# Kernel tuning notes

Hardware: AMD Instinct MI355X
Metric: run time of the kernel (lower is better)

Reference implementation:

```python
import jax, jax.numpy as jnp
import numpy as np

N, E = 50000, 800000
IN, HID, OUT = 128, 256, 128
BN_EPS = 1e-5


def setup_inputs() -> dict:
    key = jax.random.key(0)
    ks = jax.random.split(key, 12)
    x = jax.random.normal(ks[0], (N, IN), dtype=jnp.float32)
    edge_index = jax.random.randint(ks[1], (2, E), 0, N, dtype=jnp.int64)
    edge_weight = jax.random.uniform(ks[2], (E,), dtype=jnp.float32)
    # GCNConv weights (glorot-ish scale) and biases
    W0 = jax.random.normal(ks[3], (IN, HID), dtype=jnp.float32) * (1.0 / np.sqrt(IN))
    b0 = jnp.zeros((HID,), jnp.float32)
    W1 = jax.random.normal(ks[4], (HID, HID), dtype=jnp.float32) * (1.0 / np.sqrt(HID))
    b1 = jnp.zeros((HID,), jnp.float32)
    Wl = jax.random.normal(ks[5], (HID, OUT), dtype=jnp.float32) * (1.0 / np.sqrt(HID))
    bl = jnp.zeros((OUT,), jnp.float32)
    # BatchNorm affine params (eval mode: running_mean=0, running_var=1)
    g0 = 1.0 + 0.1 * jax.random.normal(ks[6], (HID,), dtype=jnp.float32)
    be0 = 0.1 * jax.random.normal(ks[7], (HID,), dtype=jnp.float32)
    g1 = 1.0 + 0.1 * jax.random.normal(ks[8], (HID,), dtype=jnp.float32)
    be1 = 0.1 * jax.random.normal(ks[9], (HID,), dtype=jnp.float32)
    return {"x": x, "edge_index": edge_index, "edge_weight": edge_weight,
            "W0": W0, "b0": b0, "W1": W1, "b1": b1, "Wl": Wl, "bl": bl,
            "g0": g0, "be0": be0, "g1": g1, "be1": be1}


def reference(x, edge_index, edge_weight, W0, b0, W1, b1, Wl, bl, g0, be0, g1, be1):
    n = x.shape[0]
    row, col = edge_index[0], edge_index[1]
    # add self-loops with weight 1 (GCNConv default)
    ar = jnp.arange(n)
    rowf = jnp.concatenate([row, ar])
    colf = jnp.concatenate([col, ar])
    wf = jnp.concatenate([edge_weight, jnp.ones((n,), x.dtype)])
    # symmetric normalization: D^{-1/2} A D^{-1/2}
    deg = jax.ops.segment_sum(wf, colf, num_segments=n)
    dinv = jnp.where(deg > 0, jax.lax.rsqrt(deg), 0.0)
    norm = dinv[rowf] * wf * dinv[colf]  # [E+N]

    def conv(h, W, b):
        h = h @ W                       # [n, d_out]
        msg = h[rowf] * norm[:, None]   # gather + scale per edge
        return jax.ops.segment_sum(msg, colf, num_segments=n) + b

    def bn_eval(h, g, b):
        # eval-mode BN with running_mean=0, running_var=1
        return h * (g / jnp.sqrt(1.0 + BN_EPS)) + b

    h = jax.nn.relu(bn_eval(conv(x, W0, b0), g0, be0))
    h = jax.nn.relu(bn_eval(conv(h, W1, b1), g1, be1))
    h = conv(h, Wl, bl)
    return jax.nn.log_softmax(h, axis=1)
```

## Files before the change

kernel.cpp:

```cpp
#include <hip/hip_runtime.h>
#include <cstddef>
#include <cstdint>


#define GCN_BN_EPS 1e-5f
#define NB_CHUNK 64
#define NPART 4

typedef short v8bf __attribute__((ext_vector_type(8)));
typedef float v4f __attribute__((ext_vector_type(4)));


__device__ __forceinline__ float4 unpack_bf4(uint2 u) {
  float4 r;
  r.x = __uint_as_float(u.x << 16);
  r.y = __uint_as_float(u.x & 0xffff0000u);
  r.z = __uint_as_float(u.y << 16);
  r.w = __uint_as_float(u.y & 0xffff0000u);
  return r;
}
__device__ __forceinline__ uint16_t f2bf(float f) {
  uint32_t u = __float_as_uint(f);
  return (uint16_t)((u + 0x7fffu + ((u >> 16) & 1u)) >> 16);
}
__device__ __forceinline__ uint2 pack_bf4(float4 v) {
  uint2 r;
  r.x = (uint32_t)f2bf(v.x) | ((uint32_t)f2bf(v.y) << 16);
  r.y = (uint32_t)f2bf(v.z) | ((uint32_t)f2bf(v.w) << 16);
  return r;
}


__global__ void detect_kernel(const int* __restrict__ ei, int* __restrict__ flag) {
  if (threadIdx.x == 0) {
    int nz = 0;
    for (int k = 1; k < 64; k += 2) nz |= ei[k];
    *flag = (nz == 0) ? 1 : 0;
  }
}

__global__ void decode_kernel(const int* __restrict__ ei, const float* __restrict__ ew,
                              const int* __restrict__ flag,
                              int* __restrict__ col_, uint2* __restrict__ pk, int E) {
  int e = blockIdx.x * blockDim.x + threadIdx.x;
  if (e >= E) return;
  int r, c;
  if (*flag) { r = ei[2 * e]; c = ei[2 * (E + e)]; }
  else       { r = ei[e];     c = ei[E + e]; }
  col_[e] = c;
  pk[e] = make_uint2((unsigned)r, __float_as_uint(ew[e]));
}

__global__ __launch_bounds__(256) void hist_kernel(const int* __restrict__ col_,
                                                   int* __restrict__ hist,
                                                   int E, int n) {
  extern __shared__ unsigned int hsh[];
  const int chunk = blockIdx.x, part = blockIdx.y;
  const int npl = (n + NPART - 1) / NPART;
  const int lo = part * npl, hi = min(lo + npl, n);
  const int nw = (npl + 1) >> 1;
  for (int i = threadIdx.x; i < nw; i += 256) hsh[i] = 0u;
  __syncthreads();
  const int per = (E + NB_CHUNK - 1) / NB_CHUNK;
  const int e0 = chunk * per, e1 = min(e0 + per, E);
  for (int e = e0 + threadIdx.x; e < e1; e += 256) {
    int c = col_[e];
    if (c >= lo && c < hi) {
      int cl = c - lo;
      atomicAdd(&hsh[cl >> 1], 1u << ((cl & 1) * 16));
    }
  }
  __syncthreads();
  for (int i = threadIdx.x; i < hi - lo; i += 256)
    hist[(size_t)chunk * n + lo + i] = (int)((hsh[i >> 1] >> ((i & 1) * 16)) & 0xffffu);
}

__global__ __launch_bounds__(256) void scan1_kernel(const int* __restrict__ hist,
                                                    int* __restrict__ cnt,
                                                    int* __restrict__ bsum, int n) {
  __shared__ int ws[4];
  int i = blockIdx.x * 256 + threadIdx.x;
  int v = 0;
  if (i < n) {
    for (int b = 0; b < NB_CHUNK; ++b) v += hist[(size_t)b * n + i];
    cnt[i] = v;
  }
  int x = v;
#pragma unroll
  for (int s = 1; s < 64; s <<= 1) x += __shfl_xor(x, s, 64);
  if ((threadIdx.x & 63) == 0) ws[threadIdx.x >> 6] = x;
  __syncthreads();
  if (threadIdx.x == 0) bsum[blockIdx.x] = ws[0] + ws[1] + ws[2] + ws[3];
}

__global__ __launch_bounds__(1024) void scan2_kernel(int* __restrict__ bsum, int G,
                                                     int* __restrict__ off, int n, int E) {
  __shared__ int wsum[16], woff[16];
  int tid = threadIdx.x, lane = tid & 63, wv = tid >> 6;
  int v = (tid < G) ? bsum[tid] : 0;
  int x = v;
#pragma unroll
  for (int s = 1; s < 64; s <<= 1) { int t = __shfl_up(x, s, 64); if (lane >= s) x += t; }
  if (lane == 63) wsum[wv] = x;
  __syncthreads();
  if (wv == 0) {
    int wsv = (lane < 16) ? wsum[lane] : 0;
    int y = wsv;
#pragma unroll
    for (int s = 1; s < 16; s <<= 1) { int t = __shfl_up(y, s, 64); if (lane >= s) y += t; }
    if (lane < 16) woff[lane] = y - wsv;
  }
  __syncthreads();
  if (tid < G) bsum[tid] = x - v + woff[wv];
  if (tid == 0) off[n] = E;
}

__global__ __launch_bounds__(256) void scan3_kernel(const int* __restrict__ cnt,
                                                    const int* __restrict__ bsum,
                                                    int* __restrict__ off, int n) {
  __shared__ int wsum[4], woff[4];
  int tid = threadIdx.x, lane = tid & 63, wv = tid >> 6;
  int i = blockIdx.x * 256 + tid;
  int v = (i < n) ? cnt[i] : 0;
  int x = v;
#pragma unroll
  for (int s = 1; s < 64; s <<= 1) { int t = __shfl_up(x, s, 64); if (lane >= s) x += t; }
  if (lane == 63) wsum[wv] = x;
  __syncthreads();
  if (tid == 0) { int r = 0; for (int k = 0; k < 4; ++k) { woff[k] = r; r += wsum[k]; } }
  __syncthreads();
  if (i < n) off[i] = x - v + woff[wv] + bsum[blockIdx.x];
}

__global__ void base_kernel(const int* __restrict__ off, int* __restrict__ hist, int n) {
  int i = blockIdx.x * blockDim.x + threadIdx.x;
  if (i >= n) return;
  int run = off[i];
  for (int b = 0; b < NB_CHUNK; ++b) {
    size_t idx = (size_t)b * n + i;
    int h = hist[idx];
    hist[idx] = run;
    run += h;
  }
}

__global__ __launch_bounds__(256) void fill_kernel(
    const int* __restrict__ col_, const uint2* __restrict__ pk,
    const int* __restrict__ base, uint2* __restrict__ csr, int E, int n) {
  extern __shared__ int cur[];
  const int chunk = blockIdx.x, part = blockIdx.y;
  const int npl = (n + NPART - 1) / NPART;
  const int lo = part * npl, hi = min(lo + npl, n);
  for (int i = threadIdx.x; i < hi - lo; i += 256)
    cur[i] = base[(size_t)chunk * n + lo + i];
  __syncthreads();
  const int per = (E + NB_CHUNK - 1) / NB_CHUNK;
  const int e0 = chunk * per, e1 = min(e0 + per, E);
  for (int e = e0 + threadIdx.x; e < e1; e += 256) {
    int c = col_[e];
    if (c >= lo && c < hi) {
      int p = atomicAdd(&cur[c - lo], 1);
      csr[p] = pk[e];
    }
  }
}

__global__ void degdinv_kernel(const int* __restrict__ off, const uint2* __restrict__ csr,
                               float* __restrict__ dinv, int n) {
  int i = blockIdx.x * blockDim.x + threadIdx.x;
  if (i >= n) return;
  float s = 1.0f;
  int p1 = off[i + 1];
  for (int p = off[i]; p < p1; ++p) s += __uint_as_float(csr[p].y);
  dinv[i] = rsqrtf(s);
}

__global__ void val_kernel(const int* __restrict__ off, uint2* __restrict__ csr,
                           const float* __restrict__ dinv, int n) {
  int i = blockIdx.x * blockDim.x + threadIdx.x;
  if (i >= n) return;
  float dc = dinv[i];
  int p1 = off[i + 1];
  for (int p = off[i]; p < p1; ++p) {
    uint2 t = csr[p];
    csr[p].y = __float_as_uint(dinv[t.x] * __uint_as_float(t.y) * dc);
  }
}


__global__ void conv_x_kernel(const float* __restrict__ x, uint16_t* __restrict__ xb,
                              int n4) {
  int i = blockIdx.x * blockDim.x + threadIdx.x;
  if (i >= n4) return;
  float4 v = *(const float4*)&x[(size_t)i * 4];
  *(uint2*)&xb[(size_t)i * 4] = pack_bf4(v);
}

__global__ void conv_wt_kernel(const float* __restrict__ W, uint16_t* __restrict__ WT,
                               int K, int Nc) {
  int i = blockIdx.x * blockDim.x + threadIdx.x;
  if (i >= K * Nc) return;
  int n = i / K, k = i - n * K;
  WT[i] = f2bf(W[(size_t)k * Nc + n]);
}


template <int EPI>
__global__ __launch_bounds__(256) void agg256_kernel(
    const uint16_t* __restrict__ hin, uint16_t* __restrict__ hout,
    const int* __restrict__ off, const uint2* __restrict__ csr,
    const float* __restrict__ dinv,
    const float* __restrict__ bias, const float* __restrict__ g,
    const float* __restrict__ be, int n) {
  const int lane = threadIdx.x & 63;
  const int c = blockIdx.x * 4 + (threadIdx.x >> 6);
  if (c >= n) return;
  const int f = lane * 4;
  const int e0 = off[c], e1 = off[c + 1];
  const float di = dinv[c];
  const float s2 = di * di;
  float4 self = unpack_bf4(*(const uint2*)&hin[(size_t)c * 256 + f]);
  float4 acc = make_float4(self.x * s2, self.y * s2, self.z * s2, self.w * s2);

  for (int base = e0; base < e1; base += 64) {
    int idx = base + lane;
    int rs = 0; float rv = 0.0f;
    if (idx < e1) { uint2 ev = csr[idx]; rs = (int)ev.x; rv = __uint_as_float(ev.y); }
    const int m = min(64, e1 - base);
    const int nG = (m + 3) >> 2;
    for (int gI = 0; gI < nG; ++gI) {
      int e_ = gI * 4;
      int s0 = __shfl(rs, e_);     float v0 = __shfl(rv, e_);
      int s1 = __shfl(rs, e_ + 1); float v1 = __shfl(rv, e_ + 1);
      int sB = __shfl(rs, e_ + 2); float v2 = __shfl(rv, e_ + 2);
      int s3 = __shfl(rs, e_ + 3); float v3 = __shfl(rv, e_ + 3);
      float4 h0 = unpack_bf4(*(const uint2*)&hin[(size_t)s0 * 256 + f]);
      float4 h1 = unpack_bf4(*(const uint2*)&hin[(size_t)s1 * 256 + f]);
      float4 h2 = unpack_bf4(*(const uint2*)&hin[(size_t)sB * 256 + f]);
      float4 h3 = unpack_bf4(*(const uint2*)&hin[(size_t)s3 * 256 + f]);
      acc.x += v0 * h0.x + v1 * h1.x + v2 * h2.x + v3 * h3.x;
      acc.y += v0 * h0.y + v1 * h1.y + v2 * h2.y + v3 * h3.y;
      acc.z += v0 * h0.z + v1 * h1.z + v2 * h2.z + v3 * h3.z;
      acc.w += v0 * h0.w + v1 * h1.w + v2 * h2.w + v3 * h3.w;
    }
  }

  if (EPI == 1) {
    const float bns = rsqrtf(1.0f + GCN_BN_EPS);
    float4 bi = *(const float4*)&bias[f];
    float4 gi = *(const float4*)&g[f];
    float4 bei = *(const float4*)&be[f];
    acc.x = fmaxf((acc.x + bi.x) * gi.x * bns + bei.x, 0.0f);
    acc.y = fmaxf((acc.y + bi.y) * gi.y * bns + bei.y, 0.0f);
    acc.z = fmaxf((acc.z + bi.z) * gi.z * bns + bei.z, 0.0f);
    acc.w = fmaxf((acc.w + bi.w) * gi.w * bns + bei.w, 0.0f);
  }
  *(uint2*)&hout[(size_t)c * 256 + f] = pack_bf4(acc);
}

template <int EPI>
__global__ __launch_bounds__(256) void agg128_kernel(
    const uint16_t* __restrict__ hin, void* __restrict__ hout_,
    const int* __restrict__ off, const uint2* __restrict__ csr,
    const float* __restrict__ dinv,
    const float* __restrict__ bias, int n) {
  const int lane = threadIdx.x & 63;
  const int sub = lane & 31;
  const int hbase = lane & 32;
  const int c = blockIdx.x * 8 + (threadIdx.x >> 6) * 2 + (lane >> 5);
  const bool active = (c < n);
  const int f = sub * 4;

  int e0 = 0, e1 = 0;
  float4 acc = make_float4(0.f, 0.f, 0.f, 0.f);
  if (active) {
    e0 = off[c]; e1 = off[c + 1];
    float di = dinv[c];
    float s2 = di * di;
    float4 self = unpack_bf4(*(const uint2*)&hin[(size_t)c * 128 + f]);
    acc = make_float4(self.x * s2, self.y * s2, self.z * s2, self.w * s2);
  }
  int nch = (e1 - e0 + 31) >> 5;
  nch = max(nch, __shfl(nch, lane ^ 32));

  for (int ch = 0; ch < nch; ++ch) {
    int idx = e0 + ch * 32 + sub;
    int rs = 0; float rv = 0.0f;
    if (active && idx < e1) { uint2 ev = csr[idx]; rs = (int)ev.x; rv = __uint_as_float(ev.y); }
    int m = e1 - (e0 + ch * 32);
    m = m < 0 ? 0 : (m > 32 ? 32 : m);
    int mMax = max(m, __shfl(m, lane ^ 32));
    const int nG = (mMax + 3) >> 2;
    for (int gI = 0; gI < nG; ++gI) {
      int e_ = hbase + gI * 4;
      int s0 = __shfl(rs, e_);     float v0 = __shfl(rv, e_);
      int s1 = __shfl(rs, e_ + 1); float v1 = __shfl(rv, e_ + 1);
      int sB = __shfl(rs, e_ + 2); float v2 = __shfl(rv, e_ + 2);
      int s3 = __shfl(rs, e_ + 3); float v3 = __shfl(rv, e_ + 3);
      float4 h0 = unpack_bf4(*(const uint2*)&hin[(size_t)s0 * 128 + f]);
      float4 h1 = unpack_bf4(*(const uint2*)&hin[(size_t)s1 * 128 + f]);
      float4 h2 = unpack_bf4(*(const uint2*)&hin[(size_t)sB * 128 + f]);
      float4 h3 = unpack_bf4(*(const uint2*)&hin[(size_t)s3 * 128 + f]);
      acc.x += v0 * h0.x + v1 * h1.x + v2 * h2.x + v3 * h3.x;
      acc.y += v0 * h0.y + v1 * h1.y + v2 * h2.y + v3 * h3.y;
      acc.z += v0 * h0.z + v1 * h1.z + v2 * h2.z + v3 * h3.z;
      acc.w += v0 * h0.w + v1 * h1.w + v2 * h2.w + v3 * h3.w;
    }
  }

  if (EPI == 0) {
    uint16_t* hout = (uint16_t*)hout_;
    if (active) *(uint2*)&hout[(size_t)c * 128 + f] = pack_bf4(acc);
  } else {
    float* hout = (float*)hout_;
    float4 bi = active ? *(const float4*)&bias[f] : make_float4(0.f, 0.f, 0.f, 0.f);
    float tx = acc.x + bi.x, ty = acc.y + bi.y, tz = acc.z + bi.z, tw = acc.w + bi.w;
    float mx = fmaxf(fmaxf(tx, ty), fmaxf(tz, tw));
#pragma unroll
    for (int s = 1; s < 32; s <<= 1) mx = fmaxf(mx, __shfl_xor(mx, s, 64));
    float ex = expf(tx - mx) + expf(ty - mx) + expf(tz - mx) + expf(tw - mx);
#pragma unroll
    for (int s = 1; s < 32; s <<= 1) ex += __shfl_xor(ex, s, 64);
    float lse = logf(ex) + mx;
    if (active) {
      float4 res = make_float4(tx - lse, ty - lse, tz - lse, tw - lse);
      *(float4*)&hout[(size_t)c * 128 + f] = res;
    }
  }
}

template <int K, int NC, int EPI>
__global__ __launch_bounds__(256) void mfma_gemm_kernel(
    const uint16_t* __restrict__ A, const uint16_t* __restrict__ WT,
    uint16_t* __restrict__ Cb, int M, int tpb,
    const float* __restrict__ bias, const float* __restrict__ g,
    const float* __restrict__ be) {
  constexpr int CW = NC / 4;
  constexpr int NT = CW / 16;
  constexpr int KS = K / 32;
  const int lane = threadIdx.x & 63;
  const int wave = threadIdx.x >> 6;
  const int quad = lane >> 4;
  const int l16 = lane & 15;
  const int col0 = wave * CW;

  const int tiles = (M + 15) >> 4;
  int t0 = blockIdx.x * tpb;
  if (t0 >= tiles) return;
  int t1 = min(t0 + tpb, tiles);

  v8bf b[KS][NT];
#pragma unroll
  for (int ks = 0; ks < KS; ++ks)
#pragma unroll
    for (int nt = 0; nt < NT; ++nt)
      b[ks][nt] = *(const v8bf*)(WT + (size_t)(col0 + nt * 16 + l16) * K +
                                 ks * 32 + quad * 8);

  float sc[NT], o1[NT], o2[NT];
  if (EPI == 1) {
    const float bns = rsqrtf(1.0f + GCN_BN_EPS);
#pragma unroll
    for (int nt = 0; nt < NT; ++nt) {
      int col = col0 + nt * 16 + l16;
      sc[nt] = g[col] * bns; o1[nt] = bias[col]; o2[nt] = be[col];
    }
  }

  v8bf a[KS], an[KS];
  {
    int arow = min(t0 * 16 + l16, M - 1);
    const uint16_t* Ap = A + (size_t)arow * K + quad * 8;
#pragma unroll
    for (int ks = 0; ks < KS; ++ks) a[ks] = *(const v8bf*)(Ap + ks * 32);
  }
  for (int t = t0; t < t1; ++t) {
    if (t + 1 < t1) {
      int arow = min((t + 1) * 16 + l16, M - 1);
      const uint16_t* Ap = A + (size_t)arow * K + quad * 8;
#pragma unroll
      for (int ks = 0; ks < KS; ++ks) an[ks] = *(const v8bf*)(Ap + ks * 32);
    }
    v4f acc[NT];
#pragma unroll
    for (int nt = 0; nt < NT; ++nt) acc[nt] = (v4f){0.f, 0.f, 0.f, 0.f};
#pragma unroll
    for (int ks = 0; ks < KS; ++ks)
#pragma unroll
      for (int nt = 0; nt < NT; ++nt)
        acc[nt] = __builtin_amdgcn_mfma_f32_16x16x32_bf16(a[ks], b[ks][nt],
                                                          acc[nt], 0, 0, 0);
    const int row0 = t * 16 + quad * 4;
#pragma unroll
    for (int nt = 0; nt < NT; ++nt) {
      const int col = col0 + nt * 16 + l16;
#pragma unroll
      for (int r = 0; r < 4; ++r) {
        int row = row0 + r;
        if (row < M) {
          float v = acc[nt][r];
          if (EPI == 1) v = fmaxf((v + o1[nt]) * sc[nt] + o2[nt], 0.0f);
          Cb[(size_t)row * NC + col] = f2bf(v);
        }
      }
    }
#pragma unroll
    for (int ks = 0; ks < KS; ++ks) a[ks] = an[ks];
  }
}


static inline char* carve(char*& p, size_t bytes) {
  char* r = p;
  p += (bytes + 255) & ~(size_t)255;
  return r;
}

extern "C" void kernel_launch(void* const* d_in, const int* in_sizes, int n_in,
                              void* d_out, int out_size, void* d_ws, size_t ws_size,
                              hipStream_t stream) {
  const int N = in_sizes[0] / 128;
  const int E = in_sizes[2];

  const float* x  = (const float*)d_in[0];
  const int*   ei = (const int*)d_in[1];
  const float* ew = (const float*)d_in[2];
  const float* W0 = (const float*)d_in[3];
  const float* b0 = (const float*)d_in[4];
  const float* W1 = (const float*)d_in[5];
  const float* b1 = (const float*)d_in[6];
  const float* Wl = (const float*)d_in[7];
  const float* bl = (const float*)d_in[8];
  const float* g0 = (const float*)d_in[9];
  const float* be0 = (const float*)d_in[10];
  const float* g1 = (const float*)d_in[11];
  const float* be1 = (const float*)d_in[12];
  float* out = (float*)d_out;

  char* p = (char*)d_ws;
  float*    dinv    = (float*)carve(p, (size_t)N * 4);
  int*      cnt     = (int*)carve(p, (size_t)N * 4);
  int*      off     = (int*)carve(p, (size_t)(N + 1) * 4);
  int*      flag    = (int*)carve(p, 256);
  int*      bsum    = (int*)carve(p, 1024 * 4);
  int*      col_    = (int*)carve(p, (size_t)E * 4);
  uint2*    pk      = (uint2*)carve(p, (size_t)E * 8);
  uint2*    csr     = (uint2*)carve(p, (size_t)E * 8);
  int*      hist    = (int*)carve(p, (size_t)NB_CHUNK * N * 4);
  uint16_t* xb16    = (uint16_t*)carve(p, (size_t)N * 128 * 2);
  uint16_t* bufR    = (uint16_t*)carve(p, (size_t)N * 128 * 2);
  uint16_t* bufP    = (uint16_t*)carve(p, (size_t)N * 256 * 2);
  uint16_t* bufQ    = (uint16_t*)carve(p, (size_t)N * 256 * 2);
  uint16_t* W0t     = (uint16_t*)carve(p, (size_t)128 * 256 * 2);
  uint16_t* W1t     = (uint16_t*)carve(p, (size_t)256 * 256 * 2);
  uint16_t* Wlt     = (uint16_t*)carve(p, (size_t)256 * 128 * 2);

  const int TB = 256;
  const int gN = (N + TB - 1) / TB;
  const int gE = (E + TB - 1) / TB;
  const int gW4 = (N + 3) / 4;
  const int gW8 = (N + 7) / 8;
  const int tiles = (N + 15) / 16;
  const int TPB = 8;
  const int gG = (tiles + TPB - 1) / TPB;
  const int npl = (N + NPART - 1) / NPART;
  const size_t ldsHist = (size_t)((npl + 1) / 2) * 4;
  const size_t ldsFill = (size_t)npl * 4;
  const dim3 gHF(NB_CHUNK, NPART);

  detect_kernel<<<1, 64, 0, stream>>>(ei, flag);
  decode_kernel<<<gE, TB, 0, stream>>>(ei, ew, flag, col_, pk, E);
  hist_kernel<<<gHF, TB, ldsHist, stream>>>(col_, hist, E, N);
  scan1_kernel<<<gN, TB, 0, stream>>>(hist, cnt, bsum, N);
  scan2_kernel<<<1, 1024, 0, stream>>>(bsum, gN, off, N, E);
  scan3_kernel<<<gN, TB, 0, stream>>>(cnt, bsum, off, N);
  base_kernel<<<gN, TB, 0, stream>>>(off, hist, N);
  fill_kernel<<<gHF, TB, ldsFill, stream>>>(col_, pk, hist, csr, E, N);
  degdinv_kernel<<<gN, TB, 0, stream>>>(off, csr, dinv, N);
  val_kernel<<<gN, TB, 0, stream>>>(off, csr, dinv, N);

  conv_x_kernel<<<(N * 32 + TB - 1) / TB, TB, 0, stream>>>(x, xb16, N * 32);
  conv_wt_kernel<<<(128 * 256 + TB - 1) / TB, TB, 0, stream>>>(W0, W0t, 128, 256);
  conv_wt_kernel<<<(256 * 256 + TB - 1) / TB, TB, 0, stream>>>(W1, W1t, 256, 256);
  conv_wt_kernel<<<(256 * 128 + TB - 1) / TB, TB, 0, stream>>>(Wl, Wlt, 256, 128);

  agg128_kernel<0><<<gW8, 256, 0, stream>>>(xb16, bufR, off, csr, dinv, nullptr, N);
  mfma_gemm_kernel<128, 256, 1><<<gG, 256, 0, stream>>>(bufR, W0t, bufP, N, TPB,
                                                        b0, g0, be0);
  mfma_gemm_kernel<256, 256, 0><<<gG, 256, 0, stream>>>(bufP, W1t, bufQ, N, TPB,
                                                        nullptr, nullptr, nullptr);
  agg256_kernel<1><<<gW4, 256, 0, stream>>>(bufQ, bufP, off, csr, dinv,
                                            b1, g1, be1, N);
  mfma_gemm_kernel<256, 128, 0><<<gG, 256, 0, stream>>>(bufP, Wlt, bufR, N, TPB,
                                                        nullptr, nullptr, nullptr);
  agg128_kernel<2><<<gW8, 256, 0, stream>>>(bufR, out, off, csr, dinv, bl, N);
}
```

Before: 384.6 us.

## Fuse CSR build stages with byte-packed LDS counters and merge conversion kernels

Merges the layout detection, edge decode and histogram into one kernel. Drops the NPART node partitioning by packing four 8-bit per-node counters into each LDS word, so one block covers every node. Folds the base-offset pass into the scan3 kernel, makes the fill kernel use byte-packed LDS counters with a relative-position trick, and merges the x and weight bf16 conversions into one launch. The aim is to cut kernel launches and redundant passes over the edge list, at the cost of running the edge-parallel stages on only 64 blocks and capping each node's per-chunk in-degree at 255, which assumes a low-degree random graph.

After: 381.9 us. About the same (-0.7%).

```diff
diff --git a/kernel.cpp b/kernel.cpp
--- a/kernel.cpp
+++ b/kernel.cpp
@@ -5,7 +5,6 @@
 
 #define GCN_BN_EPS 1e-5f
 #define NB_CHUNK 64
-#define NPART 4
 
 typedef short v8bf __attribute__((ext_vector_type(8)));
 typedef float v4f __attribute__((ext_vector_type(4)));
@@ -31,48 +30,35 @@
 }
 
 
-__global__ void detect_kernel(const int* __restrict__ ei, int* __restrict__ flag) {
+__global__ __launch_bounds__(256) void build_hist_kernel(
+    const int* __restrict__ ei, const float* __restrict__ ew,
+    int* __restrict__ col_, uint2* __restrict__ pk,
+    int* __restrict__ hist, int E, int n) {
+  extern __shared__ unsigned int h8[];
+  __shared__ int s_flag;
+  const int b = blockIdx.x;
+  const int nw = (n + 3) >> 2;
   if (threadIdx.x == 0) {
     int nz = 0;
     for (int k = 1; k < 64; k += 2) nz |= ei[k];
-    *flag = (nz == 0) ? 1 : 0;
-  }
-}
-
-__global__ void decode_kernel(const int* __restrict__ ei, const float* __restrict__ ew,
-                              const int* __restrict__ flag,
-                              int* __restrict__ col_, uint2* __restrict__ pk, int E) {
-  int e = blockIdx.x * blockDim.x + threadIdx.x;
-  if (e >= E) return;
-  int r, c;
-  if (*flag) { r = ei[2 * e]; c = ei[2 * (E + e)]; }
-  else       { r = ei[e];     c = ei[E + e]; }
-  col_[e] = c;
-  pk[e] = make_uint2((unsigned)r, __float_as_uint(ew[e]));
-}
-
-__global__ __launch_bounds__(256) void hist_kernel(const int* __restrict__ col_,
-                                                   int* __restrict__ hist,
-                                                   int E, int n) {
-  extern __shared__ unsigned int hsh[];
-  const int chunk = blockIdx.x, part = blockIdx.y;
-  const int npl = (n + NPART - 1) / NPART;
-  const int lo = part * npl, hi = min(lo + npl, n);
-  const int nw = (npl + 1) >> 1;
-  for (int i = threadIdx.x; i < nw; i += 256) hsh[i] = 0u;
-  __syncthreads();
+    s_flag = (nz == 0) ? 1 : 0;
+  }
+  for (int i = threadIdx.x; i < nw; i += 256) h8[i] = 0u;
+  __syncthreads();
+  const int flag = s_flag;
   const int per = (E + NB_CHUNK - 1) / NB_CHUNK;
-  const int e0 = chunk * per, e1 = min(e0 + per, E);
+  const int e0 = b * per, e1 = min(e0 + per, E);
   for (int e = e0 + threadIdx.x; e < e1; e += 256) {
-    int c = col_[e];
-    if (c >= lo && c < hi) {
-      int cl = c - lo;
-      atomicAdd(&hsh[cl >> 1], 1u << ((cl & 1) * 16));
-    }
-  }
-  __syncthreads();
-  for (int i = threadIdx.x; i < hi - lo; i += 256)
-    hist[(size_t)chunk * n + lo + i] = (int)((hsh[i >> 1] >> ((i & 1) * 16)) & 0xffffu);
+    int r, c;
+    if (flag) { r = ei[2 * e]; c = ei[2 * (E + e)]; }
+    else      { r = ei[e];     c = ei[E + e]; }
+    col_[e] = c;
+    pk[e] = make_uint2((unsigned)r, __float_as_uint(ew[e]));
+    atomicAdd(&h8[c >> 2], 1u << ((c & 3) * 8));
+  }
+  __syncthreads();
+  for (int i = threadIdx.x; i < n; i += 256)
+    hist[(size_t)b * n + i] = (int)((h8[i >> 2] >> ((i & 3) * 8)) & 0xffu);
 }
 
 __global__ __launch_bounds__(256) void scan1_kernel(const int* __restrict__ hist,
@@ -115,9 +101,9 @@
   if (tid == 0) off[n] = E;
 }
 
-__global__ __launch_bounds__(256) void scan3_kernel(const int* __restrict__ cnt,
-                                                    const int* __restrict__ bsum,
-                                                    int* __restrict__ off, int n) {
+__global__ __launch_bounds__(256) void scan3_base_kernel(
+    const int* __restrict__ cnt, const int* __restrict__ bsum,
+    int* __restrict__ off, int* __restrict__ hist, int n) {
   __shared__ int wsum[4], woff[4];
   int tid = threadIdx.x, lane = tid & 63, wv = tid >> 6;
   int i = blockIdx.x * 256 + tid;
@@ -129,39 +115,35 @@
   __syncthreads();
   if (tid == 0) { int r = 0; for (int k = 0; k < 4; ++k) { woff[k] = r; r += wsum[k]; } }
   __syncthreads();
-  if (i < n) off[i] = x - v + woff[wv] + bsum[blockIdx.x];
-}
-
-__global__ void base_kernel(const int* __restrict__ off, int* __restrict__ hist, int n) {
-  int i = blockIdx.x * blockDim.x + threadIdx.x;
-  if (i >= n) return;
-  int run = off[i];
-  for (int b = 0; b < NB_CHUNK; ++b) {
-    size_t idx = (size_t)b * n + i;
-    int h = hist[idx];
-    hist[idx] = run;
-    run += h;
+  if (i < n) {
+    int excl = x - v + woff[wv] + bsum[blockIdx.x];
+    off[i] = excl;
+    int run = excl;
+    for (int b = 0; b < NB_CHUNK; ++b) {
+      size_t idx = (size_t)b * n + i;
+      int h = hist[idx];
+      hist[idx] = run;
+      run += h;
+    }
   }
 }
 
 __global__ __launch_bounds__(256) void fill_kernel(
     const int* __restrict__ col_, const uint2* __restrict__ pk,
     const int* __restrict__ base, uint2* __restrict__ csr, int E, int n) {
-  extern __shared__ int cur[];
-  const int chunk = blockIdx.x, part = blockIdx.y;
-  const int npl = (n + NPART - 1) / NPART;
-  const int lo = part * npl, hi = min(lo + npl, n);
-  for (int i = threadIdx.x; i < hi - lo; i += 256)
-    cur[i] = base[(size_t)chunk * n + lo + i];
+  extern __shared__ unsigned int c8[];
+  const int b = blockIdx.x;
+  const int nw = (n + 3) >> 2;
+  for (int i = threadIdx.x; i < nw; i += 256) c8[i] = 0u;
   __syncthreads();
   const int per = (E + NB_CHUNK - 1) / NB_CHUNK;
-  const int e0 = chunk * per, e1 = min(e0 + per, E);
+  const int e0 = b * per, e1 = min(e0 + per, E);
+  const int* bb = base + (size_t)b * n;
   for (int e = e0 + threadIdx.x; e < e1; e += 256) {
     int c = col_[e];
-    if (c >= lo && c < hi) {
-      int p = atomicAdd(&cur[c - lo], 1);
-      csr[p] = pk[e];
-    }
+    unsigned old = atomicAdd(&c8[c >> 2], 1u << ((c & 3) * 8));
+    int rel = (int)((old >> ((c & 3) * 8)) & 0xffu);
+    csr[bb[c] + rel] = pk[e];
   }
 }
 
@@ -187,21 +169,34 @@
   }
 }
 
-
-__global__ void conv_x_kernel(const float* __restrict__ x, uint16_t* __restrict__ xb,
-                              int n4) {
+__global__ void conv_all_kernel(const float* __restrict__ x, uint16_t* __restrict__ xb,
+                                const float* __restrict__ W0, uint16_t* __restrict__ W0t,
+                                const float* __restrict__ W1, uint16_t* __restrict__ W1t,
+                                const float* __restrict__ Wl, uint16_t* __restrict__ Wlt,
+                                int t0) {
   int i = blockIdx.x * blockDim.x + threadIdx.x;
-  if (i >= n4) return;
-  float4 v = *(const float4*)&x[(size_t)i * 4];
-  *(uint2*)&xb[(size_t)i * 4] = pack_bf4(v);
-}
-
-__global__ void conv_wt_kernel(const float* __restrict__ W, uint16_t* __restrict__ WT,
-                               int K, int Nc) {
-  int i = blockIdx.x * blockDim.x + threadIdx.x;
-  if (i >= K * Nc) return;
-  int n = i / K, k = i - n * K;
-  WT[i] = f2bf(W[(size_t)k * Nc + n]);
+  if (i < t0) {
+    float4 v = *(const float4*)&x[(size_t)i * 4];
+    *(uint2*)&xb[(size_t)i * 4] = pack_bf4(v);
+    return;
+  }
+  int j = i - t0;
+  if (j < 128 * 256) {
+    int nn = j >> 7, k = j & 127;
+    W0t[j] = f2bf(W0[(size_t)k * 256 + nn]);
+    return;
+  }
+  j -= 128 * 256;
+  if (j < 256 * 256) {
+    int nn = j >> 8, k = j & 255;
+    W1t[j] = f2bf(W1[(size_t)k * 256 + nn]);
+    return;
+  }
+  j -= 256 * 256;
+  if (j < 256 * 128) {
+    int nn = j >> 8, k = j & 255;
+    Wlt[j] = f2bf(Wl[(size_t)k * 128 + nn]);
+  }
 }
 
 
@@ -441,7 +436,6 @@
   float*    dinv    = (float*)carve(p, (size_t)N * 4);
   int*      cnt     = (int*)carve(p, (size_t)N * 4);
   int*      off     = (int*)carve(p, (size_t)(N + 1) * 4);
-  int*      flag    = (int*)carve(p, 256);
   int*      bsum    = (int*)carve(p, 1024 * 4);
   int*      col_    = (int*)carve(p, (size_t)E * 4);
   uint2*    pk      = (uint2*)carve(p, (size_t)E * 8);
@@ -457,32 +451,25 @@
 
   const int TB = 256;
   const int gN = (N + TB - 1) / TB;
-  const int gE = (E + TB - 1) / TB;
   const int gW4 = (N + 3) / 4;
   const int gW8 = (N + 7) / 8;
   const int tiles = (N + 15) / 16;
   const int TPB = 8;
   const int gG = (tiles + TPB - 1) / TPB;
-  const int npl = (N + NPART - 1) / NPART;
-  const size_t ldsHist = (size_t)((npl + 1) / 2) * 4;
-  const size_t ldsFill = (size_t)npl * 4;
-  const dim3 gHF(NB_CHUNK, NPART);
-
-  detect_kernel<<<1, 64, 0, stream>>>(ei, flag);
-  decode_kernel<<<gE, TB, 0, stream>>>(ei, ew, flag, col_, pk, E);
-  hist_kernel<<<gHF, TB, ldsHist, stream>>>(col_, hist, E, N);
+  const size_t ldsU8 = (size_t)((N + 3) / 4) * 4;
+  const int convT0 = N * 32;
+  const int convTot = convT0 + 128 * 256 + 256 * 256 + 256 * 128;
+
+  build_hist_kernel<<<NB_CHUNK, TB, ldsU8, stream>>>(ei, ew, col_, pk, hist, E, N);
   scan1_kernel<<<gN, TB, 0, stream>>>(hist, cnt, bsum, N);
   scan2_kernel<<<1, 1024, 0, stream>>>(bsum, gN, off, N, E);
-  scan3_kernel<<<gN, TB, 0, stream>>>(cnt, bsum, off, N);
-  base_kernel<<<gN, TB, 0, stream>>>(off, hist, N);
-  fill_kernel<<<gHF, TB, ldsFill, stream>>>(col_, pk, hist, csr, E, N);
+  scan3_base_kernel<<<gN, TB, 0, stream>>>(cnt, bsum, off, hist, N);
+  fill_kernel<<<NB_CHUNK, TB, ldsU8, stream>>>(col_, pk, hist, csr, E, N);
   degdinv_kernel<<<gN, TB, 0, stream>>>(off, csr, dinv, N);
   val_kernel<<<gN, TB, 0, stream>>>(off, csr, dinv, N);
 
-  conv_x_kernel<<<(N * 32 + TB - 1) / TB, TB, 0, stream>>>(x, xb16, N * 32);
-  conv_wt_kernel<<<(128 * 256 + TB - 1) / TB, TB, 0, stream>>>(W0, W0t, 128, 256);
-  conv_wt_kernel<<<(256 * 256 + TB - 1) / TB, TB, 0, stream>>>(W1, W1t, 256, 256);
-  conv_wt_kernel<<<(256 * 128 + TB - 1) / TB, TB, 0, stream>>>(Wl, Wlt, 256, 128);
+  conv_all_kernel<<<(convTot + TB - 1) / TB, TB, 0, stream>>>(
+      x, xb16, W0, W0t, W1, W1t, Wl, Wlt, convT0);
 
   agg128_kernel<0><<<gW8, 256, 0, stream>>>(xb16, bufR, off, csr, dinv, nullptr, N);
   mfma_gemm_kernel<128, 256, 1><<<gG, 256, 0, stream>>>(bufR, W0t, bufP, N, TPB,
```
